# Kernel tuning notes

Hardware: AMD Instinct MI355X
Metric: run time of the kernel (lower is better)

The kernel has to match this reference:

```python
import jax, jax.numpy as jnp
import numpy as np

N = 100000        # number of nodes
E = 3200000       # number of edges (avg degree 32)
D_IN = 256
D_OUT = 256


def setup_inputs() -> dict:
    key = jax.random.key(0)
    k_x, k_w, k_r, k_c, k_v = jax.random.split(key, 5)
    x = jax.random.normal(k_x, (N, D_IN), dtype=jnp.float32)
    # nn.Linear weight, stored torch-style as (out_features, in_features)
    W = jax.random.normal(k_w, (D_OUT, D_IN), dtype=jnp.float32) / np.sqrt(D_IN)
    edge_row = jax.random.randint(k_r, (E,), 0, N, dtype=jnp.int32)
    edge_col = jax.random.randint(k_c, (E,), 0, N, dtype=jnp.int32)
    edge_val = jax.random.uniform(k_v, (E,), dtype=jnp.float32)
    return {"x": x, "W": W, "edge_row": edge_row, "edge_col": edge_col,
            "edge_val": edge_val}


def reference(x, W, edge_row, edge_col, edge_val):
    # support = X @ W^T  (torch nn.Linear, no bias), computed in float32
    support = jnp.einsum('nd,od->no', x.astype(jnp.float32), W.astype(jnp.float32))
    # SpMM: out[i] = sum_{e: row[e]==i} val[e] * support[col[e]]
    gathered = edge_val.astype(jnp.float32)[:, None] * support[edge_col]  # [E, D_OUT]
    out = jax.ops.segment_sum(gathered, edge_row, num_segments=N)        # [N, D_OUT]
    return out
```

## Files before the change

### kernel.cpp

```cpp
#include <hip/hip_runtime.h>

#define N_NODES 100000
#define N_EDGES 3200000
#define D 256

#define NBKT 782
#define BCAP 4608
#define P1_BLOCKS 782
#define CVT_BLOCKS 64

using bf16x8 = __attribute__((ext_vector_type(8))) short;
using f32x4  = __attribute__((ext_vector_type(4))) float;
using i32x4  = __attribute__((ext_vector_type(4))) int;
using i32x2  = __attribute__((ext_vector_type(2))) int;

__device__ inline float bf2f(unsigned short b) {
    union { unsigned u; float f; } v; v.u = ((unsigned)b) << 16; return v.f;
}
__device__ inline unsigned short f2bf(float f) {
    union { float f; unsigned u; } v; v.f = f;
    unsigned u = v.u;
    u += 0x7FFFu + ((u >> 16) & 1u);
    return (unsigned short)(u >> 16);
}

__global__ __launch_bounds__(256) void prep(const float* __restrict__ W,
                                            unsigned short* __restrict__ wb,
                                            int* __restrict__ bucket_next) {
    int bid = blockIdx.x;
    if (bid < CVT_BLOCKS) {
        int i = (bid * 256 + threadIdx.x) * 4;
        float4 f = *(const float4*)(W + i);
        ushort4 o;
        o.x = f2bf(f.x); o.y = f2bf(f.y); o.z = f2bf(f.z); o.w = f2bf(f.w);
        *(ushort4*)(wb + i) = o;
    } else {
        int t = (bid - CVT_BLOCKS) * 256 + threadIdx.x;
        if (t < NBKT) bucket_next[t] = t * BCAP;
    }
}

__global__ __launch_bounds__(256) void gemm_part(
    const float* __restrict__ x,
    const unsigned short* __restrict__ wb,
    unsigned short* __restrict__ sb,
    const i32x4* __restrict__ erow4,
    const i32x4* __restrict__ ecol4,
    const f32x4* __restrict__ eval4,
    int* __restrict__ bucket_next,
    i32x2* __restrict__ bkt)
{
    __shared__ int h_cnt[NBKT];
    __shared__ int h_base[NBKT];
    int bid = blockIdx.x;
    int r3 = bid % 3, g3 = bid / 3;
    if (r3 == 0) {
        int p = g3;
        int tid = threadIdx.x;
        for (int i = tid; i < NBKT; i += 256) h_cnt[i] = 0;
        __syncthreads();
        int e0 = p * 4096;
        int jmax = (N_EDGES - e0) >> 10; if (jmax > 4) jmax = 4;
        int w0[4][4], w1[4][4], bs[4][4];
#pragma unroll
        for (int j = 0; j < 4; ++j) {
            if (j < jmax) {
                int q = p * 1024 + j * 256 + tid;
                i32x4 r4 = __builtin_nontemporal_load(erow4 + q);
                i32x4 c4 = __builtin_nontemporal_load(ecol4 + q);
                f32x4 v4 = __builtin_nontemporal_load(eval4 + q);
#pragma unroll
                for (int k = 0; k < 4; ++k) {
                    int row = r4[k];
                    int b   = row >> 7;
                    int rl  = row & 127;
                    int slot = atomicAdd(&h_cnt[b], 1);
                    w0[j][k] = c4[k] | (rl << 24);
                    w1[j][k] = __float_as_int(v4[k]);
                    bs[j][k] = (b << 13) | slot;
                }
            }
        }
        __syncthreads();
        for (int i = tid; i < NBKT; i += 256)
            h_base[i] = atomicAdd(&bucket_next[i], h_cnt[i]);
        __syncthreads();
#pragma unroll
        for (int j = 0; j < 4; ++j) {
            if (j < jmax) {
#pragma unroll
                for (int k = 0; k < 4; ++k) {
                    int b    = bs[j][k] >> 13;
                    int slot = bs[j][k] & 8191;
                    int dst  = h_base[b] + slot;
                    if (dst < (b + 1) * BCAP) {
                        i32x2 o; o[0] = w0[j][k]; o[1] = w1[j][k];
                        bkt[dst] = o;
                    }
                }
            }
        }
        return;
    }
    int g = 2 * g3 + (r3 - 1);
    int wave = g * 4 + (int)(threadIdx.x >> 6);
    int m0 = wave << 4;
    if (m0 >= N_NODES) return;
    int lane = threadIdx.x & 63;
    int quad = lane >> 4;
    int r16  = lane & 15;

    const f32x4* arow = (const f32x4*)(x + (size_t)(m0 + r16) * D + quad * 8);
    const unsigned short* bbase = wb + (size_t)r16 * D + quad * 8;

    f32x4 acc[16];
#pragma unroll
    for (int t = 0; t < 16; ++t) acc[t] = (f32x4){0.f, 0.f, 0.f, 0.f};

    for (int k0 = 0; k0 < D; k0 += 32) {
        f32x4 fa0 = __builtin_nontemporal_load(arow + (k0 >> 2));
        f32x4 fa1 = __builtin_nontemporal_load(arow + (k0 >> 2) + 1);
        bf16x8 a;
        a[0] = (short)f2bf(fa0[0]); a[1] = (short)f2bf(fa0[1]);
        a[2] = (short)f2bf(fa0[2]); a[3] = (short)f2bf(fa0[3]);
        a[4] = (short)f2bf(fa1[0]); a[5] = (short)f2bf(fa1[1]);
        a[6] = (short)f2bf(fa1[2]); a[7] = (short)f2bf(fa1[3]);
#pragma unroll
        for (int t = 0; t < 16; ++t) {
            bf16x8 b = *(const bf16x8*)(bbase + (size_t)t * 16 * D + k0);
            acc[t] = __builtin_amdgcn_mfma_f32_16x16x32_bf16(b, a, acc[t], 0, 0, 0);
        }
    }

#pragma unroll
    for (int t = 0; t < 16; ++t) {
        ushort4 o;
        o.x = f2bf(acc[t][0]); o.y = f2bf(acc[t][1]);
        o.z = f2bf(acc[t][2]); o.w = f2bf(acc[t][3]);
        *(ushort4*)(sb + (size_t)(m0 + r16) * D + t * 16 + quad * 4) = o;
    }
}

__global__ __launch_bounds__(512) void csr_spmm(
    const int* __restrict__ bucket_next,
    const i32x2* __restrict__ bkt,
    const unsigned short* __restrict__ sb, float* __restrict__ out)
{
    __shared__ int2 lds_e[BCAP];
    __shared__ int cnt[128], scn[128], cur[128];
    int b = blockIdx.x, tid = threadIdx.x;
    int base = b * BCAP;
    int ne = bucket_next[b] - base; if (ne > BCAP) ne = BCAP;

    if (tid < 128) cnt[tid] = 0;
    __syncthreads();
    for (int idx = tid; idx < ne; idx += 512) {
        i32x2 e = bkt[base + idx];
        atomicAdd(&cnt[((unsigned)e[0]) >> 24], 1);
    }
    __syncthreads();
    if (tid < 128) scn[tid] = cnt[tid];
    __syncthreads();
    for (int off = 1; off < 128; off <<= 1) {
        int v = 0;
        if (tid < 128 && tid >= off) v = scn[tid - off];
        __syncthreads();
        if (tid < 128) scn[tid] += v;
        __syncthreads();
    }
    if (tid < 128) { int ex = scn[tid] - cnt[tid]; scn[tid] = ex; cur[tid] = ex; }
    __syncthreads();
    for (int idx = tid; idx < ne; idx += 512) {
        i32x2 e = bkt[base + idx];
        int rl  = ((unsigned)e[0]) >> 24;
        int pos = atomicAdd(&cur[rl], 1);
        lds_e[pos] = make_int2(e[0] & 0x00FFFFFF, e[1]);
    }
    __syncthreads();

    int wid = tid >> 6, lane = tid & 63, hi = lane >> 5;
    const unsigned short* basep = sb + (size_t)(lane & 31) * 8;

#define PAIR(AA, BB, EE) do {                                        \
        int2 pa = lds_e[EE];                                         \
        int2 pb = lds_e[(EE) + 1];                                   \
        int   col = hi ? pb.x : pa.x;                                \
        float v   = __int_as_float(hi ? pb.y : pa.y);                \
        bf16x8 s = *(const bf16x8*)(basep + ((size_t)col << 8));     \
        AA[0] += v * bf2f((unsigned short)s[0]);                     \
        AA[1] += v * bf2f((unsigned short)s[1]);                     \
        AA[2] += v * bf2f((unsigned short)s[2]);                     \
        AA[3] += v * bf2f((unsigned short)s[3]);                     \
        BB[0] += v * bf2f((unsigned short)s[4]);                     \
        BB[1] += v * bf2f((unsigned short)s[5]);                     \
        BB[2] += v * bf2f((unsigned short)s[6]);                     \
        BB[3] += v * bf2f((unsigned short)s[7]);                     \
    } while (0)

    for (int r = 0; r < 16; ++r) {
        int rl  = wid * 16 + r;
        int row = (b << 7) + rl;
        if (row >= N_NODES) break;
        int e   = scn[rl];
        int end = cur[rl];

        f32x4 a0 = {0.f,0.f,0.f,0.f}, b0 = {0.f,0.f,0.f,0.f};
        f32x4 a1 = {0.f,0.f,0.f,0.f}, b1 = {0.f,0.f,0.f,0.f};
        f32x4 a2 = {0.f,0.f,0.f,0.f}, b2 = {0.f,0.f,0.f,0.f};
        f32x4 a3 = {0.f,0.f,0.f,0.f}, b3 = {0.f,0.f,0.f,0.f};

        for (; e + 8 <= end; e += 8) {
            PAIR(a0, b0, e);
            PAIR(a1, b1, e + 2);
            PAIR(a2, b2, e + 4);
            PAIR(a3, b3, e + 6);
        }
        for (; e + 2 <= end; e += 2) PAIR(a0, b0, e);
        if (e < end) {
            int2 pa = lds_e[e];
            int   col = pa.x;
            float v   = hi ? 0.f : __int_as_float(pa.y);
            bf16x8 s = *(const bf16x8*)(basep + ((size_t)col << 8));
            a0[0] += v * bf2f((unsigned short)s[0]);
            a0[1] += v * bf2f((unsigned short)s[1]);
            a0[2] += v * bf2f((unsigned short)s[2]);
            a0[3] += v * bf2f((unsigned short)s[3]);
            b0[0] += v * bf2f((unsigned short)s[4]);
            b0[1] += v * bf2f((unsigned short)s[5]);
            b0[2] += v * bf2f((unsigned short)s[6]);
            b0[3] += v * bf2f((unsigned short)s[7]);
        }

        f32x4 A = (a0 + a1) + (a2 + a3);
        f32x4 B = (b0 + b1) + (b2 + b3);
#pragma unroll
        for (int j = 0; j < 4; ++j) {
            A[j] += __shfl_xor(A[j], 32);
            B[j] += __shfl_xor(B[j], 32);
        }
        if (lane < 32) {
            float* o = out + (size_t)row * D + lane * 8;
            __builtin_nontemporal_store(A, (f32x4*)o);
            __builtin_nontemporal_store(B, (f32x4*)(o + 4));
        }
    }
#undef PAIR
}

extern "C" void kernel_launch(void* const* d_in, const int* in_sizes, int n_in,
                              void* d_out, int out_size, void* d_ws, size_t ws_size,
                              hipStream_t stream) {
    const float* x    = (const float*)d_in[0];
    const float* W    = (const float*)d_in[1];
    const int*   erow = (const int*)d_in[2];
    const int*   ecol = (const int*)d_in[3];
    const float* eval = (const float*)d_in[4];
    float* out = (float*)d_out;

    char* ws = (char*)d_ws;
    unsigned short* wb    = (unsigned short*)(ws + 0);
    unsigned short* sb    = (unsigned short*)(ws + 131072);
    int*            bnext = (int*)(ws + 51331072);
    i32x2*          bkt   = (i32x2*)(ws + 51335168);

    prep<<<CVT_BLOCKS + 4, 256, 0, stream>>>(W, wb, bnext);

    gemm_part<<<3 * P1_BLOCKS, 256, 0, stream>>>(
        x, wb, sb, (const i32x4*)erow, (const i32x4*)ecol, (const f32x4*)eval,
        bnext, bkt);

    csr_spmm<<<NBKT, 512, 0, stream>>>(bnext, bkt, sb, out);
}
```

Baseline: 565.6 us.

## Split fused GEMM/partition kernel into separate GEMM and two-pass partition kernels

Separates the interleaved GEMM and edge-bucketing work, previously one combined launch, into a standalone GEMM kernel and a 1024-thread partition kernel. The partition kernel now reads row indices twice, once for the histogram and once for the scatter, instead of holding all edges in registers. The GEMM preloads all 16 B fragments before the MFMAs and drops the nontemporal loads. This removes the overlap between the compute-bound GEMM and the memory-bound partition and adds an extra launch, in exchange for lower register pressure and simpler scheduling. Within a bucket, edge order now depends on atomic timing.

```diff
diff --git a/kernel.cpp b/kernel.cpp
--- a/kernel.cpp
+++ b/kernel.cpp
@@ -6,7 +6,8 @@
 
 #define NBKT 782
 #define BCAP 4608
-#define P1_BLOCKS 782
+#define PART_BLOCKS 196
+#define GEMM_BLOCKS 1564
 #define CVT_BLOCKS 64
 
 using bf16x8 = __attribute__((ext_vector_type(8))) short;
@@ -40,10 +41,52 @@
     }
 }
 
-__global__ __launch_bounds__(256) void gemm_part(
+__global__ __launch_bounds__(256) void gemm(
     const float* __restrict__ x,
     const unsigned short* __restrict__ wb,
-    unsigned short* __restrict__ sb,
+    unsigned short* __restrict__ sb)
+{
+    int wave = blockIdx.x * 4 + (int)(threadIdx.x >> 6);
+    int m0 = wave << 4;
+    if (m0 >= N_NODES) return;
+    int lane = threadIdx.x & 63;
+    int quad = lane >> 4;
+    int r16  = lane & 15;
+
+    const f32x4* arow = (const f32x4*)(x + (size_t)(m0 + r16) * D + quad * 8);
+    const unsigned short* bbase = wb + (size_t)r16 * D + quad * 8;
+
+    f32x4 acc[16];
+#pragma unroll
+    for (int t = 0; t < 16; ++t) acc[t] = (f32x4){0.f, 0.f, 0.f, 0.f};
+
+    for (int k0 = 0; k0 < D; k0 += 32) {
+        f32x4 fa0 = *(arow + (k0 >> 2));
+        f32x4 fa1 = *(arow + (k0 >> 2) + 1);
+        bf16x8 bf[16];
+#pragma unroll
+        for (int t = 0; t < 16; ++t)
+            bf[t] = *(const bf16x8*)(bbase + (size_t)t * 16 * D + k0);
+        bf16x8 a;
+        a[0] = (short)f2bf(fa0[0]); a[1] = (short)f2bf(fa0[1]);
+        a[2] = (short)f2bf(fa0[2]); a[3] = (short)f2bf(fa0[3]);
+        a[4] = (short)f2bf(fa1[0]); a[5] = (short)f2bf(fa1[1]);
+        a[6] = (short)f2bf(fa1[2]); a[7] = (short)f2bf(fa1[3]);
+#pragma unroll
+        for (int t = 0; t < 16; ++t)
+            acc[t] = __builtin_amdgcn_mfma_f32_16x16x32_bf16(bf[t], a, acc[t], 0, 0, 0);
+    }
+
+#pragma unroll
+    for (int t = 0; t < 16; ++t) {
+        ushort4 o;
+        o.x = f2bf(acc[t][0]); o.y = f2bf(acc[t][1]);
+        o.z = f2bf(acc[t][2]); o.w = f2bf(acc[t][3]);
+        *(ushort4*)(sb + (size_t)(m0 + r16) * D + t * 16 + quad * 4) = o;
+    }
+}
+
+__global__ __launch_bounds__(1024) void part(
     const i32x4* __restrict__ erow4,
     const i32x4* __restrict__ ecol4,
     const f32x4* __restrict__ eval4,
@@ -51,93 +94,43 @@
     i32x2* __restrict__ bkt)
 {
     __shared__ int h_cnt[NBKT];
-    __shared__ int h_base[NBKT];
-    int bid = blockIdx.x;
-    int r3 = bid % 3, g3 = bid / 3;
-    if (r3 == 0) {
-        int p = g3;
-        int tid = threadIdx.x;
-        for (int i = tid; i < NBKT; i += 256) h_cnt[i] = 0;
-        __syncthreads();
-        int e0 = p * 4096;
-        int jmax = (N_EDGES - e0) >> 10; if (jmax > 4) jmax = 4;
-        int w0[4][4], w1[4][4], bs[4][4];
-#pragma unroll
-        for (int j = 0; j < 4; ++j) {
-            if (j < jmax) {
-                int q = p * 1024 + j * 256 + tid;
-                i32x4 r4 = __builtin_nontemporal_load(erow4 + q);
-                i32x4 c4 = __builtin_nontemporal_load(ecol4 + q);
-                f32x4 v4 = __builtin_nontemporal_load(eval4 + q);
-#pragma unroll
-                for (int k = 0; k < 4; ++k) {
-                    int row = r4[k];
-                    int b   = row >> 7;
-                    int rl  = row & 127;
-                    int slot = atomicAdd(&h_cnt[b], 1);
-                    w0[j][k] = c4[k] | (rl << 24);
-                    w1[j][k] = __float_as_int(v4[k]);
-                    bs[j][k] = (b << 13) | slot;
+    int p = blockIdx.x, tid = threadIdx.x;
+    for (int i = tid; i < NBKT; i += 1024) h_cnt[i] = 0;
+    __syncthreads();
+    int q0 = p * 4096;
+#pragma unroll
+    for (int j = 0; j < 4; ++j) {
+        int q = q0 + j * 1024 + tid;
+        if (q < N_EDGES / 4) {
+            i32x4 r4 = erow4[q];
+#pragma unroll
+            for (int k = 0; k < 4; ++k)
+                atomicAdd(&h_cnt[r4[k] >> 7], 1);
+        }
+    }
+    __syncthreads();
+    for (int i = tid; i < NBKT; i += 1024)
+        h_cnt[i] = atomicAdd(&bucket_next[i], h_cnt[i]);
+    __syncthreads();
+#pragma unroll
+    for (int j = 0; j < 4; ++j) {
+        int q = q0 + j * 1024 + tid;
+        if (q < N_EDGES / 4) {
+            i32x4 r4 = erow4[q];
+            i32x4 c4 = ecol4[q];
+            f32x4 v4 = eval4[q];
+#pragma unroll
+            for (int k = 0; k < 4; ++k) {
+                int row = r4[k];
+                int b   = row >> 7;
+                int dst = atomicAdd(&h_cnt[b], 1);
+                if (dst < (b + 1) * BCAP) {
+                    i32x2 o; o[0] = c4[k] | ((row & 127) << 24);
+                    o[1] = __float_as_int(v4[k]);
+                    bkt[dst] = o;
                 }
             }
         }
-        __syncthreads();
-        for (int i = tid; i < NBKT; i += 256)
-            h_base[i] = atomicAdd(&bucket_next[i], h_cnt[i]);
-        __syncthreads();
-#pragma unroll
-        for (int j = 0; j < 4; ++j) {
-            if (j < jmax) {
-#pragma unroll
-                for (int k = 0; k < 4; ++k) {
-                    int b    = bs[j][k] >> 13;
-                    int slot = bs[j][k] & 8191;
-                    int dst  = h_base[b] + slot;
-                    if (dst < (b + 1) * BCAP) {
-                        i32x2 o; o[0] = w0[j][k]; o[1] = w1[j][k];
-                        bkt[dst] = o;
-                    }
-                }
-            }
-        }
-        return;
-    }
-    int g = 2 * g3 + (r3 - 1);
-    int wave = g * 4 + (int)(threadIdx.x >> 6);
-    int m0 = wave << 4;
-    if (m0 >= N_NODES) return;
-    int lane = threadIdx.x & 63;
-    int quad = lane >> 4;
-    int r16  = lane & 15;
-
-    const f32x4* arow = (const f32x4*)(x + (size_t)(m0 + r16) * D + quad * 8);
-    const unsigned short* bbase = wb + (size_t)r16 * D + quad * 8;
-
-    f32x4 acc[16];
-#pragma unroll
-    for (int t = 0; t < 16; ++t) acc[t] = (f32x4){0.f, 0.f, 0.f, 0.f};
-
-    for (int k0 = 0; k0 < D; k0 += 32) {
-        f32x4 fa0 = __builtin_nontemporal_load(arow + (k0 >> 2));
-        f32x4 fa1 = __builtin_nontemporal_load(arow + (k0 >> 2) + 1);
-        bf16x8 a;
-        a[0] = (short)f2bf(fa0[0]); a[1] = (short)f2bf(fa0[1]);
-        a[2] = (short)f2bf(fa0[2]); a[3] = (short)f2bf(fa0[3]);
-        a[4] = (short)f2bf(fa1[0]); a[5] = (short)f2bf(fa1[1]);
-        a[6] = (short)f2bf(fa1[2]); a[7] = (short)f2bf(fa1[3]);
-#pragma unroll
-        for (int t = 0; t < 16; ++t) {
-            bf16x8 b = *(const bf16x8*)(bbase + (size_t)t * 16 * D + k0);
-            acc[t] = __builtin_amdgcn_mfma_f32_16x16x32_bf16(b, a, acc[t], 0, 0, 0);
-        }
-    }
-
-#pragma unroll
-    for (int t = 0; t < 16; ++t) {
-        ushort4 o;
-        o.x = f2bf(acc[t][0]); o.y = f2bf(acc[t][1]);
-        o.z = f2bf(acc[t][2]); o.w = f2bf(acc[t][3]);
-        *(ushort4*)(sb + (size_t)(m0 + r16) * D + t * 16 + quad * 4) = o;
     }
 }
 
@@ -265,9 +258,10 @@
 
     prep<<<CVT_BLOCKS + 4, 256, 0, stream>>>(W, wb, bnext);
 
-    gemm_part<<<3 * P1_BLOCKS, 256, 0, stream>>>(
-        x, wb, sb, (const i32x4*)erow, (const i32x4*)ecol, (const f32x4*)eval,
-        bnext, bkt);
+    gemm<<<GEMM_BLOCKS, 256, 0, stream>>>(x, wb, sb);
+
+    part<<<PART_BLOCKS, 1024, 0, stream>>>(
+        (const i32x4*)erow, (const i32x4*)ecol, (const f32x4*)eval, bnext, bkt);
 
     csr_spmm<<<NBKT, 512, 0, stream>>>(bnext, bkt, sb, out);
 }
```

After: 574.4 us. About the same (+1.6%).
